# Kernel tuning notes

Measured on AMD Instinct MI355X. Metric: run time of the kernel, lower is better.

The kernel has to match this reference:

```python
import jax, jax.numpy as jnp
import numpy as np

GEN_DIM = 200
CON_DIM = 128
CO_DIM = 4
LATENT_DIM = 64
CI_ENC_DIM = 128
EXT_DIM = 16
CLIP = 5.0
B = 65536

GEN_IN = EXT_DIM + CO_DIM            # 20
CON_IN = 2 * CI_ENC_DIM + LATENT_DIM # 320
STATE_DIM = GEN_DIM + CON_DIM + CO_DIM + CO_DIM + (CO_DIM + EXT_DIM) + LATENT_DIM  # 420


def _gru_cell(x, h, w_ih, w_hh, b_ih, b_hh, clip):
    # torch GRUCell convention: gates ordered (r, z, n), hidden clipped (LFADS ClippedGRUCell)
    gi = x @ w_ih.T + b_ih
    gh = h @ w_hh.T + b_hh
    i_r, i_z, i_n = jnp.split(gi, 3, axis=1)
    h_r, h_z, h_n = jnp.split(gh, 3, axis=1)
    r = jax.nn.sigmoid(i_r + h_r)
    z = jax.nn.sigmoid(i_z + h_z)
    n = jnp.tanh(i_n + r * h_n)
    h_new = (1.0 - z) * n + z * h
    return jnp.clip(h_new, -clip, clip)


def setup_inputs() -> dict:
    key = jax.random.key(0)
    ks = jax.random.split(key, 14)
    def w(k, shape, fan_in):
        return (jax.random.normal(k, shape, jnp.float32) / np.sqrt(fan_in)).astype(jnp.float32)
    return {
        "x": jax.random.normal(ks[0], (B, 2 * CI_ENC_DIM + EXT_DIM), jnp.float32),
        "h0": jax.random.normal(ks[1], (B, STATE_DIM), jnp.float32),
        "eps": jax.random.normal(ks[2], (B, CO_DIM), jnp.float32),
        "gen_w_ih": w(ks[3], (3 * GEN_DIM, GEN_IN), GEN_IN),
        "gen_w_hh": w(ks[4], (3 * GEN_DIM, GEN_DIM), GEN_DIM),
        "gen_b_ih": jnp.zeros((3 * GEN_DIM,), jnp.float32),
        "gen_b_hh": jnp.zeros((3 * GEN_DIM,), jnp.float32),
        "con_w_ih": w(ks[5], (3 * CON_DIM, CON_IN), CON_IN),
        "con_w_hh": w(ks[6], (3 * CON_DIM, CON_DIM), CON_DIM),
        "con_b_ih": jnp.zeros((3 * CON_DIM,), jnp.float32),
        "con_b_hh": jnp.zeros((3 * CON_DIM,), jnp.float32),
        "co_w": w(ks[7], (2 * CO_DIM, CON_DIM), CON_DIM),
        "co_b": jnp.zeros((2 * CO_DIM,), jnp.float32),
        "fac_w": w(ks[8], (LATENT_DIM, GEN_DIM), GEN_DIM),
    }


def reference(x, h0, eps, gen_w_ih, gen_w_hh, gen_b_ih, gen_b_hh,
              con_w_ih, con_w_hh, con_b_ih, con_b_hh, co_w, co_b, fac_w):
    # split h0 per state_dims [GEN, CON, CO, CO, CO+EXT, LATENT]
    o0 = GEN_DIM
    o1 = o0 + CON_DIM
    o2 = o1 + CO_DIM
    o3 = o2 + CO_DIM
    o4 = o3 + CO_DIM + EXT_DIM
    gen_state = h0[:, :o0]
    con_state = h0[:, o0:o1]
    factor = h0[:, o4:]
    # split input per [2*CI_ENC_DIM, EXT_DIM]
    ci_step = x[:, :2 * CI_ENC_DIM]
    ext_step = x[:, 2 * CI_ENC_DIM:]

    # controller path (dropout is identity at inference)
    con_input = jnp.concatenate([ci_step, factor], axis=1)
    con_state = _gru_cell(con_input, con_state, con_w_ih, con_w_hh, con_b_ih, con_b_hh, CLIP)
    co_params = con_state @ co_w.T + co_b
    co_mean = co_params[:, :CO_DIM]
    co_logvar = co_params[:, CO_DIM:]
    co_std = jnp.exp(0.5 * co_logvar)  # sqrt(exp(logvar))
    con_output = co_mean + co_std * eps  # reparameterized rsample

    gen_input = jnp.concatenate([con_output, ext_step], axis=1)
    gen_state = _gru_cell(gen_input, gen_state, gen_w_ih, gen_w_hh, gen_b_ih, gen_b_hh, CLIP)

    # kernel-normalized linear: rows L2-normalized, no bias
    normed_w = fac_w / jnp.maximum(jnp.linalg.norm(fac_w, axis=1, keepdims=True), 1e-12)
    factor = gen_state @ normed_w.T

    hidden = jnp.concatenate([gen_state, con_state, co_mean, co_std, gen_input, factor], axis=1)
    return hidden
```

## Files before the change

kernel.cpp:

```cpp
#include <hip/hip_runtime.h>
#include <math.h>


#define NT 512
#define RT 128
#define XD 272
#define HD 420

typedef unsigned short ushort_t;
typedef __attribute__((ext_vector_type(8))) short bf8;
typedef __attribute__((ext_vector_type(4))) float f4;
typedef __attribute__((ext_vector_type(4))) unsigned short us4;

#define WS_W1 0
#define WS_W2 122880
#define WS_W3 172032
#define WS_W4 191488
#define WS_W5 327680

#define STA 328
#define STG 216
#define STH 136
#define STR3 88

#define O_A   0
#define O_GN  55296
#define O_R2  83968
#define O_R3  118784
#define POOLB 141312

__device__ __forceinline__ ushort_t f2bf(float f) {
  union { float f; unsigned u; } v; v.f = f;
  unsigned r = v.u + 0x7FFFu + ((v.u >> 16) & 1u);
  return (ushort_t)(r >> 16);
}
__device__ __forceinline__ float bf2f(ushort_t u) {
  union { unsigned u; float f; } v; v.u = ((unsigned)u) << 16; return v.f;
}
__device__ __forceinline__ us4 f2bf4(f4 v) {
  us4 b; b.x = f2bf(v.x); b.y = f2bf(v.y); b.z = f2bf(v.z); b.w = f2bf(v.w); return b;
}
__device__ __forceinline__ f4 bf2f4(us4 b) {
  f4 v; v.x = bf2f(b.x); v.y = bf2f(b.y); v.z = bf2f(b.z); v.w = bf2f(b.w); return v;
}
__device__ __forceinline__ float rcpf(float x) { return __builtin_amdgcn_rcpf(x); }
__device__ __forceinline__ float sigf(float x) {
  return rcpf(1.0f + __expf(-x));
}
__device__ __forceinline__ float tanhf_(float x) {
  return 1.0f - 2.0f * rcpf(1.0f + __expf(2.0f * x));
}

#define MFMA(a, b, c) __builtin_amdgcn_mfma_f32_16x16x32_bf16((a), (b), (c), 0, 0, 0)

__global__ void prep_w(const float* __restrict__ cw1, const float* __restrict__ cw2,
                       const float* __restrict__ gw3, const float* __restrict__ gw4,
                       ushort_t* __restrict__ ws) {
  int tid = blockIdx.x * blockDim.x + threadIdx.x;
  int np = gridDim.x * blockDim.x;
  for (int i = tid; i < 384 * 320; i += np) ws[WS_W1 + i] = f2bf(cw1[i]);
  for (int i = tid; i < 384 * 128; i += np) ws[WS_W2 + i] = f2bf(cw2[i]);
  for (int i = tid; i < 608 * 32; i += np) {
    int n = i >> 5, k = i & 31;
    ws[WS_W3 + i] = (n < 600 && k < 20) ? f2bf(gw3[n * 20 + k]) : (ushort_t)0;
  }
  for (int i = tid; i < 608 * 224; i += np) {
    int n = i / 224, k = i - n * 224;
    ws[WS_W4 + i] = (n < 600 && k < 200) ? f2bf(gw4[n * 200 + k]) : (ushort_t)0;
  }
}

__global__ void prep_fac(const float* __restrict__ fw, ushort_t* __restrict__ ws) {
  int n = blockIdx.x;
  int l = threadIdx.x;
  float ss = 0.f;
  for (int k = l; k < 200; k += 64) { float v = fw[n * 200 + k]; ss = fmaf(v, v, ss); }
  for (int off = 32; off; off >>= 1) ss += __shfl_down(ss, off, 64);
  ss = __shfl(ss, 0, 64);
  float inv = 1.0f / fmaxf(sqrtf(ss), 1e-12f);
  for (int k = l; k < 224; k += 64)
    ws[WS_W5 + n * 224 + k] = (k < 200) ? f2bf(fw[n * 200 + k] * inv) : (ushort_t)0;
}

__global__ __launch_bounds__(NT, 2) void decoder_kernel(
    const float* __restrict__ x, const float* __restrict__ h0, const float* __restrict__ eps,
    const float* __restrict__ gen_b_ih, const float* __restrict__ gen_b_hh,
    const float* __restrict__ con_b_ih, const float* __restrict__ con_b_hh,
    const float* __restrict__ co_w, const float* __restrict__ co_b,
    const ushort_t* __restrict__ ws, float* __restrict__ out)
{
  __shared__ __align__(16) unsigned char spool[POOLB];
  ushort_t* sA  = (ushort_t*)(spool + O_A);
  ushort_t* sGo = (ushort_t*)(spool + O_A);
  ushort_t* sGn = (ushort_t*)(spool + O_GN);
  ushort_t* sR2 = (ushort_t*)(spool + O_R2);
  ushort_t* sR3 = (ushort_t*)(spool + O_R3);

  const int tid = threadIdx.x;
  const int rbase = blockIdx.x * RT;
  const int lane = tid & 63;
  const int w = tid >> 6;
  const int bn = lane & 15;
  const int kq = (lane >> 4) << 3;
  const int qrow = (lane >> 4) << 2;

  #pragma unroll
  for (int it = 0; it < 16; ++it) {
    int idx = tid + it * NT;
    int r = idx >> 6, c4 = (idx & 63) << 2;
    f4 v = *(const f4*)&x[(size_t)(rbase + r) * XD + c4];
    *(us4*)&sA[r * STA + c4] = f2bf4(v);
  }
  {
    int r = tid >> 2, e = (tid & 3) << 2;
    f4 v = *(const f4*)&x[(size_t)(rbase + r) * XD + 256 + e];
    *(us4*)&sR3[r * STR3 + 4 + e] = f2bf4(v);
  }
  #pragma unroll
  for (int it = 0; it < 8; ++it) {
    int idx = tid + it * NT;
    int r = idx >> 5, c4 = (idx & 31) << 2;
    f4 v = *(const f4*)&h0[(size_t)(rbase + r) * HD + 200 + c4];
    *(us4*)&sR2[r * STH + c4] = f2bf4(v);
  }
  #pragma unroll
  for (int it = 0; it < 4; ++it) {
    int idx = tid + it * NT;
    int r = idx >> 4, c4 = (idx & 15) << 2;
    f4 v = *(const f4*)&h0[(size_t)(rbase + r) * HD + 356 + c4];
    *(us4*)&sA[r * STA + 256 + c4] = f2bf4(v);
  }
  if (tid < 384) {
    int r = tid / 3, q = (tid - (tid / 3) * 3) << 2;
    us4 z = {0, 0, 0, 0};
    *(us4*)&sR3[r * STR3 + 20 + q] = z;
  }
  __syncthreads();

  const int col = (w << 4) + bn;

  f4 aR[8], aZ[8], aN[8], aHN[8];
  #pragma unroll
  for (int ri = 0; ri < 8; ++ri) {
    aR[ri] = (f4){0.f, 0.f, 0.f, 0.f};
    aZ[ri] = (f4){0.f, 0.f, 0.f, 0.f};
    aN[ri] = (f4){0.f, 0.f, 0.f, 0.f};
    aHN[ri] = (f4){0.f, 0.f, 0.f, 0.f};
  }
  {
    const ushort_t* W2 = ws + WS_W2;
    const ushort_t* W1 = ws + WS_W1;
    bf8 w2f[4][3], w1a[5][3];
    #pragma unroll
    for (int k = 0; k < 4; ++k) {
      w2f[k][0] = *(const bf8*)&W2[(size_t)(col) * 128 + k * 32 + kq];
      w2f[k][1] = *(const bf8*)&W2[(size_t)(128 + col) * 128 + k * 32 + kq];
      w2f[k][2] = *(const bf8*)&W2[(size_t)(256 + col) * 128 + k * 32 + kq];
    }
    #pragma unroll
    for (int k = 0; k < 5; ++k) {
      w1a[k][0] = *(const bf8*)&W1[(size_t)(col) * 320 + k * 32 + kq];
      w1a[k][1] = *(const bf8*)&W1[(size_t)(128 + col) * 320 + k * 32 + kq];
      w1a[k][2] = *(const bf8*)&W1[(size_t)(256 + col) * 320 + k * 32 + kq];
    }
    #pragma unroll
    for (int k = 0; k < 4; ++k) {
      #pragma unroll
      for (int ri = 0; ri < 8; ++ri) {
        bf8 a = *(const bf8*)&sR2[(ri * 16 + bn) * STH + k * 32 + kq];
        aR[ri] = MFMA(a, w2f[k][0], aR[ri]);
        aZ[ri] = MFMA(a, w2f[k][1], aZ[ri]);
        aHN[ri] = MFMA(a, w2f[k][2], aHN[ri]);
      }
    }
    bf8 w1b[5][3];
    #pragma unroll
    for (int k = 0; k < 5; ++k) {
      w1b[k][0] = *(const bf8*)&W1[(size_t)(col) * 320 + (k + 5) * 32 + kq];
      w1b[k][1] = *(const bf8*)&W1[(size_t)(128 + col) * 320 + (k + 5) * 32 + kq];
      w1b[k][2] = *(const bf8*)&W1[(size_t)(256 + col) * 320 + (k + 5) * 32 + kq];
    }
    #pragma unroll
    for (int k = 0; k < 5; ++k) {
      #pragma unroll
      for (int ri = 0; ri < 8; ++ri) {
        bf8 a = *(const bf8*)&sA[(ri * 16 + bn) * STA + k * 32 + kq];
        aR[ri] = MFMA(a, w1a[k][0], aR[ri]);
        aZ[ri] = MFMA(a, w1a[k][1], aZ[ri]);
        aN[ri] = MFMA(a, w1a[k][2], aN[ri]);
      }
    }
    #pragma unroll
    for (int k = 0; k < 5; ++k) {
      #pragma unroll
      for (int ri = 0; ri < 8; ++ri) {
        bf8 a = *(const bf8*)&sA[(ri * 16 + bn) * STA + (k + 5) * 32 + kq];
        aR[ri] = MFMA(a, w1b[k][0], aR[ri]);
        aZ[ri] = MFMA(a, w1b[k][1], aZ[ri]);
        aN[ri] = MFMA(a, w1b[k][2], aN[ri]);
      }
    }
  }
  __syncthreads();

  for (int idx = tid; idx < 128 * 54; idx += NT) {
    int r = idx / 54, u = idx - (idx / 54) * 54;
    if (u < 50) {
      f4 v = *(const f4*)&h0[(size_t)(rbase + r) * HD + (u << 2)];
      *(us4*)&sGo[r * STG + (u << 2)] = f2bf4(v);
    } else {
      us4 z = {0, 0, 0, 0};
      *(us4*)&sGo[r * STG + 200 + ((u - 50) << 2)] = z;
    }
  }
  {
    float brr = con_b_ih[col] + con_b_hh[col];
    float brz = con_b_ih[128 + col] + con_b_hh[128 + col];
    float bin = con_b_ih[256 + col], bhn = con_b_hh[256 + col];
    #pragma unroll
    for (int ri = 0; ri < 8; ++ri) {
      #pragma unroll
      for (int j = 0; j < 4; ++j) {
        int row = ri * 16 + qrow + j;
        float hold = bf2f(sR2[row * STH + col]);
        float rr = sigf(aR[ri][j] + brr);
        float zz = sigf(aZ[ri][j] + brz);
        float nn = tanhf_(aN[ri][j] + bin + rr * (aHN[ri][j] + bhn));
        float hv = (1.f - zz) * nn + zz * hold;
        hv = fminf(fmaxf(hv, -5.f), 5.f);
        sR2[row * STH + col] = f2bf(hv);
      }
    }
  }
  __syncthreads();

  {
    int cn = tid & 7;
    #pragma unroll
    for (int half = 0; half < 2; ++half) {
      int crow = (tid >> 3) + half * 64;
      float acc = co_b[cn];
      #pragma unroll 8
      for (int k0 = 0; k0 < 128; k0 += 4) {
        f4 hv = bf2f4(*(const us4*)&sR2[crow * STH + k0]);
        f4 wv = *(const f4*)&co_w[cn * 128 + k0];
        acc = fmaf(hv.x, wv.x, acc);
        acc = fmaf(hv.y, wv.y, acc);
        acc = fmaf(hv.z, wv.z, acc);
        acc = fmaf(hv.w, wv.w, acc);
      }
      float lv = __shfl(acc, lane + 4, 64);
      if (cn < 4) {
        float stdv = __expf(0.5f * lv);
        float ov = fmaf(stdv, eps[(size_t)(rbase + crow) * 4 + cn], acc);
        sR2[crow * STH + 128 + cn] = f2bf(acc);
        sR2[crow * STH + 132 + cn] = f2bf(stdv);
        sR3[crow * STR3 + cn] = f2bf(ov);
      }
    }
  }
  __syncthreads();

  for (int idx = tid; idx < 128 * 34; idx += NT) {
    int r = idx / 34, c4 = (idx - (idx / 34) * 34) << 2;
    f4 v = bf2f4(*(const us4*)&sR2[r * STH + c4]);
    *(f4*)&out[(size_t)(rbase + r) * HD + 200 + c4] = v;
  }
  __syncthreads();

  {
    int r = tid >> 2, q = (tid & 3) << 2;
    us4 z = {0, 0, 0, 0};
    *(us4*)&sGn[r * STG + 200 + q] = z;
  }
  {
    const ushort_t* W3 = ws + WS_W3;
    const ushort_t* W4 = ws + WS_W4;
    for (int t = w; t < 13; t += 8) {
      int c = (t << 4) + bn;
      bf8 w3f[3], w4a[4][3];
      w3f[0] = *(const bf8*)&W3[(size_t)(c) * 32 + kq];
      w3f[1] = *(const bf8*)&W3[(size_t)(200 + c) * 32 + kq];
      w3f[2] = *(const bf8*)&W3[(size_t)(400 + c) * 32 + kq];
      #pragma unroll
      for (int k = 0; k < 4; ++k) {
        w4a[k][0] = *(const bf8*)&W4[(size_t)(c) * 224 + k * 32 + kq];
        w4a[k][1] = *(const bf8*)&W4[(size_t)(200 + c) * 224 + k * 32 + kq];
        w4a[k][2] = *(const bf8*)&W4[(size_t)(400 + c) * 224 + k * 32 + kq];
      }
      f4 gR[8], gZ[8], gN[8], gHN[8];
      #pragma unroll
      for (int ri = 0; ri < 8; ++ri) {
        gR[ri] = (f4){0.f, 0.f, 0.f, 0.f};
        gZ[ri] = (f4){0.f, 0.f, 0.f, 0.f};
        gN[ri] = (f4){0.f, 0.f, 0.f, 0.f};
        gHN[ri] = (f4){0.f, 0.f, 0.f, 0.f};
      }
      #pragma unroll
      for (int ri = 0; ri < 8; ++ri) {
        bf8 a = *(const bf8*)&sR3[(ri * 16 + bn) * STR3 + kq];
        gR[ri] = MFMA(a, w3f[0], gR[ri]);
        gZ[ri] = MFMA(a, w3f[1], gZ[ri]);
        gN[ri] = MFMA(a, w3f[2], gN[ri]);
      }
      bf8 w4b[3][3];
      #pragma unroll
      for (int k = 0; k < 3; ++k) {
        w4b[k][0] = *(const bf8*)&W4[(size_t)(c) * 224 + (k + 4) * 32 + kq];
        w4b[k][1] = *(const bf8*)&W4[(size_t)(200 + c) * 224 + (k + 4) * 32 + kq];
        w4b[k][2] = *(const bf8*)&W4[(size_t)(400 + c) * 224 + (k + 4) * 32 + kq];
      }
      #pragma unroll
      for (int k = 0; k < 4; ++k) {
        #pragma unroll
        for (int ri = 0; ri < 8; ++ri) {
          bf8 a = *(const bf8*)&sGo[(ri * 16 + bn) * STG + k * 32 + kq];
          gR[ri] = MFMA(a, w4a[k][0], gR[ri]);
          gZ[ri] = MFMA(a, w4a[k][1], gZ[ri]);
          gHN[ri] = MFMA(a, w4a[k][2], gHN[ri]);
        }
      }
      #pragma unroll
      for (int k = 0; k < 3; ++k) {
        #pragma unroll
        for (int ri = 0; ri < 8; ++ri) {
          bf8 a = *(const bf8*)&sGo[(ri * 16 + bn) * STG + (k + 4) * 32 + kq];
          gR[ri] = MFMA(a, w4b[k][0], gR[ri]);
          gZ[ri] = MFMA(a, w4b[k][1], gZ[ri]);
          gHN[ri] = MFMA(a, w4b[k][2], gHN[ri]);
        }
      }
      if (c < 200) {
        float brr = gen_b_ih[c] + gen_b_hh[c];
        float brz = gen_b_ih[200 + c] + gen_b_hh[200 + c];
        float bin = gen_b_ih[400 + c], bhn = gen_b_hh[400 + c];
        #pragma unroll
        for (int ri = 0; ri < 8; ++ri) {
          #pragma unroll
          for (int j = 0; j < 4; ++j) {
            int row = ri * 16 + qrow + j;
            float hold = bf2f(sGo[row * STG + c]);
            float rr = sigf(gR[ri][j] + brr);
            float zz = sigf(gZ[ri][j] + brz);
            float nn = tanhf_(gN[ri][j] + bin + rr * (gHN[ri][j] + bhn));
            float hv = (1.f - zz) * nn + zz * hold;
            hv = fminf(fmaxf(hv, -5.f), 5.f);
            sGn[row * STG + c] = f2bf(hv);
          }
        }
      }
    }
  }
  __syncthreads();

  {
    const ushort_t* W5 = ws + WS_W5;
    #pragma unroll
    for (int job = 0; job < 4; ++job) {
      int ri = ((w & 3) << 1) + (job & 1);
      int ct = ((w >> 2) << 1) + (job >> 1);
      bf8 w5f[7];
      #pragma unroll
      for (int k = 0; k < 7; ++k)
        w5f[k] = *(const bf8*)&W5[(size_t)((ct << 4) + bn) * 224 + k * 32 + kq];
      f4 acc = (f4){0.f, 0.f, 0.f, 0.f};
      #pragma unroll
      for (int k = 0; k < 7; ++k) {
        bf8 a = *(const bf8*)&sGn[(ri * 16 + bn) * STG + k * 32 + kq];
        acc = MFMA(a, w5f[k], acc);
      }
      #pragma unroll
      for (int j = 0; j < 4; ++j) {
        int row = ri * 16 + qrow + j;
        sR3[row * STR3 + 20 + (ct << 4) + bn] = f2bf(acc[j]);
      }
    }
  }
  __syncthreads();

  for (int idx = tid; idx < 128 * 71; idx += NT) {
    int r = idx / 71, u = idx - (idx / 71) * 71;
    if (u < 50) {
      f4 v = bf2f4(*(const us4*)&sGn[r * STG + (u << 2)]);
      *(f4*)&out[(size_t)(rbase + r) * HD + (u << 2)] = v;
    } else {
      int u2 = u - 50;
      f4 v = bf2f4(*(const us4*)&sR3[r * STR3 + (u2 << 2)]);
      *(f4*)&out[(size_t)(rbase + r) * HD + 336 + (u2 << 2)] = v;
    }
  }
}

extern "C" void kernel_launch(void* const* d_in, const int* in_sizes, int n_in,
                              void* d_out, int out_size, void* d_ws, size_t ws_size,
                              hipStream_t stream) {
  const float* x        = (const float*)d_in[0];
  const float* h0       = (const float*)d_in[1];
  const float* eps      = (const float*)d_in[2];
  const float* gen_w_ih = (const float*)d_in[3];
  const float* gen_w_hh = (const float*)d_in[4];
  const float* gen_b_ih = (const float*)d_in[5];
  const float* gen_b_hh = (const float*)d_in[6];
  const float* con_w_ih = (const float*)d_in[7];
  const float* con_w_hh = (const float*)d_in[8];
  const float* con_b_ih = (const float*)d_in[9];
  const float* con_b_hh = (const float*)d_in[10];
  const float* co_w     = (const float*)d_in[11];
  const float* co_b     = (const float*)d_in[12];
  const float* fac_w    = (const float*)d_in[13];
  float* out = (float*)d_out;
  ushort_t* ws = (ushort_t*)d_ws;

  hipLaunchKernelGGL(prep_w, dim3(256), dim3(512), 0, stream,
                     con_w_ih, con_w_hh, gen_w_ih, gen_w_hh, ws);
  hipLaunchKernelGGL(prep_fac, dim3(64), dim3(64), 0, stream, fac_w, ws);

  int nrows = in_sizes[2] / 4;
  int grid = nrows / RT;
  hipLaunchKernelGGL(decoder_kernel, dim3(grid), dim3(NT), 0, stream,
                     x, h0, eps, gen_b_ih, gen_b_hh, con_b_ih, con_b_hh,
                     co_w, co_b, ws, out);
}
```

Measured before the change: 154.5 us.

## Double block size to 1024 threads and split rows across wave halves

Raises the decoder block from 512 to 1024 threads and gives each wave half the rows (64 instead of 128) in the controller and generator GRU MFMA phases, the co-params dot product and the factor projection. Global load loops are halved to match. This roughly halves per-thread accumulator registers and adds waves to hide latency. In exchange, each wave now loads its weight fragments for half as many rows, so weight fetch traffic per block doubles, and launch_bounds(1024,4) forces a tight register budget that may cause spilling.

```diff
diff --git a/kernel.cpp b/kernel.cpp
--- a/kernel.cpp
+++ b/kernel.cpp
@@ -2,7 +2,7 @@
 #include <math.h>
 
 
-#define NT 512
+#define NT 1024
 #define RT 128
 #define XD 272
 #define HD 420
@@ -82,7 +82,7 @@
     ws[WS_W5 + n * 224 + k] = (k < 200) ? f2bf(fw[n * 200 + k] * inv) : (ushort_t)0;
 }
 
-__global__ __launch_bounds__(NT, 2) void decoder_kernel(
+__global__ __launch_bounds__(NT, 4) void decoder_kernel(
     const float* __restrict__ x, const float* __restrict__ h0, const float* __restrict__ eps,
     const float* __restrict__ gen_b_ih, const float* __restrict__ gen_b_hh,
     const float* __restrict__ con_b_ih, const float* __restrict__ con_b_hh,
@@ -105,26 +105,26 @@
   const int qrow = (lane >> 4) << 2;
 
   #pragma unroll
-  for (int it = 0; it < 16; ++it) {
+  for (int it = 0; it < 8; ++it) {
     int idx = tid + it * NT;
     int r = idx >> 6, c4 = (idx & 63) << 2;
     f4 v = *(const f4*)&x[(size_t)(rbase + r) * XD + c4];
     *(us4*)&sA[r * STA + c4] = f2bf4(v);
   }
-  {
+  if (tid < 512) {
     int r = tid >> 2, e = (tid & 3) << 2;
     f4 v = *(const f4*)&x[(size_t)(rbase + r) * XD + 256 + e];
     *(us4*)&sR3[r * STR3 + 4 + e] = f2bf4(v);
   }
   #pragma unroll
-  for (int it = 0; it < 8; ++it) {
+  for (int it = 0; it < 4; ++it) {
     int idx = tid + it * NT;
     int r = idx >> 5, c4 = (idx & 31) << 2;
     f4 v = *(const f4*)&h0[(size_t)(rbase + r) * HD + 200 + c4];
     *(us4*)&sR2[r * STH + c4] = f2bf4(v);
   }
   #pragma unroll
-  for (int it = 0; it < 4; ++it) {
+  for (int it = 0; it < 2; ++it) {
     int idx = tid + it * NT;
     int r = idx >> 4, c4 = (idx & 15) << 2;
     f4 v = *(const f4*)&h0[(size_t)(rbase + r) * HD + 356 + c4];
@@ -137,11 +137,12 @@
   }
   __syncthreads();
 
-  const int col = (w << 4) + bn;
-
-  f4 aR[8], aZ[8], aN[8], aHN[8];
+  const int col = ((w & 7) << 4) + bn;
+  const int rb2 = (w >> 3) << 6;
+
+  f4 aR[4], aZ[4], aN[4], aHN[4];
   #pragma unroll
-  for (int ri = 0; ri < 8; ++ri) {
+  for (int ri = 0; ri < 4; ++ri) {
     aR[ri] = (f4){0.f, 0.f, 0.f, 0.f};
     aZ[ri] = (f4){0.f, 0.f, 0.f, 0.f};
     aN[ri] = (f4){0.f, 0.f, 0.f, 0.f};
@@ -166,8 +167,8 @@
     #pragma unroll
     for (int k = 0; k < 4; ++k) {
       #pragma unroll
-      for (int ri = 0; ri < 8; ++ri) {
-        bf8 a = *(const bf8*)&sR2[(ri * 16 + bn) * STH + k * 32 + kq];
+      for (int ri = 0; ri < 4; ++ri) {
+        bf8 a = *(const bf8*)&sR2[(rb2 + ri * 16 + bn) * STH + k * 32 + kq];
         aR[ri] = MFMA(a, w2f[k][0], aR[ri]);
         aZ[ri] = MFMA(a, w2f[k][1], aZ[ri]);
         aHN[ri] = MFMA(a, w2f[k][2], aHN[ri]);
@@ -183,8 +184,8 @@
     #pragma unroll
     for (int k = 0; k < 5; ++k) {
       #pragma unroll
-      for (int ri = 0; ri < 8; ++ri) {
-        bf8 a = *(const bf8*)&sA[(ri * 16 + bn) * STA + k * 32 + kq];
+      for (int ri = 0; ri < 4; ++ri) {
+        bf8 a = *(const bf8*)&sA[(rb2 + ri * 16 + bn) * STA + k * 32 + kq];
         aR[ri] = MFMA(a, w1a[k][0], aR[ri]);
         aZ[ri] = MFMA(a, w1a[k][1], aZ[ri]);
         aN[ri] = MFMA(a, w1a[k][2], aN[ri]);
@@ -193,8 +194,8 @@
     #pragma unroll
     for (int k = 0; k < 5; ++k) {
       #pragma unroll
-      for (int ri = 0; ri < 8; ++ri) {
-        bf8 a = *(const bf8*)&sA[(ri * 16 + bn) * STA + (k + 5) * 32 + kq];
+      for (int ri = 0; ri < 4; ++ri) {
+        bf8 a = *(const bf8*)&sA[(rb2 + ri * 16 + bn) * STA + (k + 5) * 32 + kq];
         aR[ri] = MFMA(a, w1b[k][0], aR[ri]);
         aZ[ri] = MFMA(a, w1b[k][1], aZ[ri]);
         aN[ri] = MFMA(a, w1b[k][2], aN[ri]);
@@ -218,10 +219,10 @@
     float brz = con_b_ih[128 + col] + con_b_hh[128 + col];
     float bin = con_b_ih[256 + col], bhn = con_b_hh[256 + col];
     #pragma unroll
-    for (int ri = 0; ri < 8; ++ri) {
+    for (int ri = 0; ri < 4; ++ri) {
       #pragma unroll
       for (int j = 0; j < 4; ++j) {
-        int row = ri * 16 + qrow + j;
+        int row = rb2 + ri * 16 + qrow + j;
         float hold = bf2f(sR2[row * STH + col]);
         float rr = sigf(aR[ri][j] + brr);
         float zz = sigf(aZ[ri][j] + brz);
@@ -235,28 +236,24 @@
   __syncthreads();
 
   {
-    int cn = tid & 7;
-    #pragma unroll
-    for (int half = 0; half < 2; ++half) {
-      int crow = (tid >> 3) + half * 64;
-      float acc = co_b[cn];
-      #pragma unroll 8
-      for (int k0 = 0; k0 < 128; k0 += 4) {
-        f4 hv = bf2f4(*(const us4*)&sR2[crow * STH + k0]);
-        f4 wv = *(const f4*)&co_w[cn * 128 + k0];
-        acc = fmaf(hv.x, wv.x, acc);
-        acc = fmaf(hv.y, wv.y, acc);
-        acc = fmaf(hv.z, wv.z, acc);
-        acc = fmaf(hv.w, wv.w, acc);
-      }
-      float lv = __shfl(acc, lane + 4, 64);
-      if (cn < 4) {
-        float stdv = __expf(0.5f * lv);
-        float ov = fmaf(stdv, eps[(size_t)(rbase + crow) * 4 + cn], acc);
-        sR2[crow * STH + 128 + cn] = f2bf(acc);
-        sR2[crow * STH + 132 + cn] = f2bf(stdv);
-        sR3[crow * STR3 + cn] = f2bf(ov);
-      }
+    int crow = tid >> 3, cn = tid & 7;
+    float acc = co_b[cn];
+    #pragma unroll 8
+    for (int k0 = 0; k0 < 128; k0 += 4) {
+      f4 hv = bf2f4(*(const us4*)&sR2[crow * STH + k0]);
+      f4 wv = *(const f4*)&co_w[cn * 128 + k0];
+      acc = fmaf(hv.x, wv.x, acc);
+      acc = fmaf(hv.y, wv.y, acc);
+      acc = fmaf(hv.z, wv.z, acc);
+      acc = fmaf(hv.w, wv.w, acc);
+    }
+    float lv = __shfl(acc, lane + 4, 64);
+    if (cn < 4) {
+      float stdv = __expf(0.5f * lv);
+      float ov = fmaf(stdv, eps[(size_t)(rbase + crow) * 4 + cn], acc);
+      sR2[crow * STH + 128 + cn] = f2bf(acc);
+      sR2[crow * STH + 132 + cn] = f2bf(stdv);
+      sR3[crow * STR3 + cn] = f2bf(ov);
     }
   }
   __syncthreads();
@@ -268,7 +265,7 @@
   }
   __syncthreads();
 
-  {
+  if (tid < 512) {
     int r = tid >> 2, q = (tid & 3) << 2;
     us4 z = {0, 0, 0, 0};
     *(us4*)&sGn[r * STG + 200 + q] = z;
@@ -276,8 +273,10 @@
   {
     const ushort_t* W3 = ws + WS_W3;
     const ushort_t* W4 = ws + WS_W4;
-    for (int t = w; t < 13; t += 8) {
-      int c = (t << 4) + bn;
+    for (int jj = w; jj < 26; jj += 16) {
+      int ct = jj >> 1;
+      int rb6 = (jj & 1) << 6;
+      int c = (ct << 4) + bn;
       bf8 w3f[3], w4a[4][3];
       w3f[0] = *(const bf8*)&W3[(size_t)(c) * 32 + kq];
       w3f[1] = *(const bf8*)&W3[(size_t)(200 + c) * 32 + kq];
@@ -288,17 +287,17 @@
         w4a[k][1] = *(const bf8*)&W4[(size_t)(200 + c) * 224 + k * 32 + kq];
         w4a[k][2] = *(const bf8*)&W4[(size_t)(400 + c) * 224 + k * 32 + kq];
       }
-      f4 gR[8], gZ[8], gN[8], gHN[8];
-      #pragma unroll
-      for (int ri = 0; ri < 8; ++ri) {
+      f4 gR[4], gZ[4], gN[4], gHN[4];
+      #pragma unroll
+      for (int ri = 0; ri < 4; ++ri) {
         gR[ri] = (f4){0.f, 0.f, 0.f, 0.f};
         gZ[ri] = (f4){0.f, 0.f, 0.f, 0.f};
         gN[ri] = (f4){0.f, 0.f, 0.f, 0.f};
         gHN[ri] = (f4){0.f, 0.f, 0.f, 0.f};
       }
       #pragma unroll
-      for (int ri = 0; ri < 8; ++ri) {
-        bf8 a = *(const bf8*)&sR3[(ri * 16 + bn) * STR3 + kq];
+      for (int ri = 0; ri < 4; ++ri) {
+        bf8 a = *(const bf8*)&sR3[(rb6 + ri * 16 + bn) * STR3 + kq];
         gR[ri] = MFMA(a, w3f[0], gR[ri]);
         gZ[ri] = MFMA(a, w3f[1], gZ[ri]);
         gN[ri] = MFMA(a, w3f[2], gN[ri]);
@@ -313,8 +312,8 @@
       #pragma unroll
       for (int k = 0; k < 4; ++k) {
         #pragma unroll
-        for (int ri = 0; ri < 8; ++ri) {
-          bf8 a = *(const bf8*)&sGo[(ri * 16 + bn) * STG + k * 32 + kq];
+        for (int ri = 0; ri < 4; ++ri) {
+          bf8 a = *(const bf8*)&sGo[(rb6 + ri * 16 + bn) * STG + k * 32 + kq];
           gR[ri] = MFMA(a, w4a[k][0], gR[ri]);
           gZ[ri] = MFMA(a, w4a[k][1], gZ[ri]);
           gHN[ri] = MFMA(a, w4a[k][2], gHN[ri]);
@@ -323,8 +322,8 @@
       #pragma unroll
       for (int k = 0; k < 3; ++k) {
         #pragma unroll
-        for (int ri = 0; ri < 8; ++ri) {
-          bf8 a = *(const bf8*)&sGo[(ri * 16 + bn) * STG + (k + 4) * 32 + kq];
+        for (int ri = 0; ri < 4; ++ri) {
+          bf8 a = *(const bf8*)&sGo[(rb6 + ri * 16 + bn) * STG + (k + 4) * 32 + kq];
           gR[ri] = MFMA(a, w4b[k][0], gR[ri]);
           gZ[ri] = MFMA(a, w4b[k][1], gZ[ri]);
           gHN[ri] = MFMA(a, w4b[k][2], gHN[ri]);
@@ -335,10 +334,10 @@
         float brz = gen_b_ih[200 + c] + gen_b_hh[200 + c];
         float bin = gen_b_ih[400 + c], bhn = gen_b_hh[400 + c];
         #pragma unroll
-        for (int ri = 0; ri < 8; ++ri) {
+        for (int ri = 0; ri < 4; ++ri) {
           #pragma unroll
           for (int j = 0; j < 4; ++j) {
-            int row = ri * 16 + qrow + j;
+            int row = rb6 + ri * 16 + qrow + j;
             float hold = bf2f(sGo[row * STG + c]);
             float rr = sigf(gR[ri][j] + brr);
             float zz = sigf(gZ[ri][j] + brz);
@@ -356,9 +355,10 @@
   {
     const ushort_t* W5 = ws + WS_W5;
     #pragma unroll
-    for (int job = 0; job < 4; ++job) {
-      int ri = ((w & 3) << 1) + (job & 1);
-      int ct = ((w >> 2) << 1) + (job >> 1);
+    for (int jj = 0; jj < 2; ++jj) {
+      int job = w + (jj << 4);
+      int ri8 = job & 7;
+      int ct = job >> 3;
       bf8 w5f[7];
       #pragma unroll
       for (int k = 0; k < 7; ++k)
@@ -366,12 +366,12 @@
       f4 acc = (f4){0.f, 0.f, 0.f, 0.f};
       #pragma unroll
       for (int k = 0; k < 7; ++k) {
-        bf8 a = *(const bf8*)&sGn[(ri * 16 + bn) * STG + k * 32 + kq];
+        bf8 a = *(const bf8*)&sGn[(ri8 * 16 + bn) * STG + k * 32 + kq];
         acc = MFMA(a, w5f[k], acc);
       }
       #pragma unroll
       for (int j = 0; j < 4; ++j) {
-        int row = ri * 16 + qrow + j;
+        int row = ri8 * 16 + qrow + j;
         sR3[row * STR3 + 20 + (ct << 4) + bn] = f2bf(acc[j]);
       }
     }
```

New measurement: 169.8 us. 9.9% more time.
